# Performance work log

Measured on AMD Instinct MI355X. Metric: run time of the kernel, lower is better.

The kernel has to match this reference:

```python
import jax, jax.numpy as jnp
import numpy as np

IN_FEAT = 3 * 299 * 299  # 268203
D1 = 512
H = 28
OUT = 2


def setup_inputs() -> dict:
    key = jax.random.key(0)
    ks = jax.random.split(key, 10)
    B, T = 4, 64
    s1 = 1.0 / np.sqrt(IN_FEAT)
    s2 = 1.0 / np.sqrt(D1)
    s3 = 1.0 / np.sqrt(H)
    return {
        "x": jax.random.normal(ks[0], (B, T, 3, 299, 299), jnp.float32),
        "W1": jax.random.uniform(ks[1], (IN_FEAT, D1), jnp.float32, -s1, s1),
        "b1": jax.random.uniform(ks[2], (D1,), jnp.float32, -s1, s1),
        "Wi": jax.random.uniform(ks[3], (D1, H), jnp.float32, -s2, s2),
        "Wr": jax.random.uniform(ks[4], (H, H), jnp.float32, -s3, s3),
        "br": jax.random.uniform(ks[5], (H,), jnp.float32, -s3, s3),
        "A": jax.random.normal(ks[6], (H,), jnp.float32),
        "tau": 1.0 + jax.random.uniform(ks[7], (H,), jnp.float32),  # positive time constants
        "W2": jax.random.uniform(ks[8], (H, OUT), jnp.float32, -s3, s3),
        "b2": jax.random.uniform(ks[9], (OUT,), jnp.float32, -s3, s3),
    }


def reference(x, W1, b1, Wi, Wr, br, A, tau, W2, b2):
    B, T = x.shape[0], x.shape[1]
    xf = x.reshape(B, T, -1)                      # [B, T, 268203]
    h1 = jax.nn.relu(jnp.einsum('btf,fd->btd', xf, W1) + b1)  # [B, T, 512]
    u = jnp.einsum('btd,dh->bth', h1, Wi)         # precomputed input drive [B, T, H]
    dt = 1.0

    def step(h, u_t):
        # fused-Euler LTC cell: f gates both time-constant and attractor A
        ft = jax.nn.sigmoid(u_t + h @ Wr + br)
        h_new = (h + dt * ft * A) / (1.0 + dt * (1.0 / tau + ft))
        return h_new, h_new

    h0 = jnp.zeros((B, H), x.dtype)
    _, hs = jax.lax.scan(step, h0, jnp.swapaxes(u, 0, 1))  # [T, B, H]
    last = jax.nn.relu(hs[-1])                    # relu then take last step
    out = last @ W2 + b2                          # [B, 2]
    return jax.nn.sigmoid(out)
```

## Files before the change

### kernel.cpp

```cpp
#include <hip/hip_runtime.h>
#include <hip/hip_bf16.h>

#define KTOT   268203
#define MROWS  256
#define NCOLS  512
#define HDIM   28
#define NSTEPS 8382
#define FSTEP  8381
#define KREM   11
#define BN     256

typedef __attribute__((ext_vector_type(4))) float  f32x4;
typedef __attribute__((ext_vector_type(8))) __bf16 bf16x8;

#define AUX_NT 2

static __device__ inline bf16x8 pack8(const float* f) {
    union { bf16x8 v; __hip_bfloat16 h[8]; } u;
    #pragma unroll
    for (int j = 0; j < 8; ++j) u.h[j] = __float2bfloat16(f[j]);
    return u.v;
}
static __device__ inline unsigned short bfbits(float v) {
    __hip_bfloat16 h = __float2bfloat16(v);
    union { __hip_bfloat16 h; unsigned short u; } c; c.h = h; return c.u;
}

__global__ __launch_bounds__(512, 2) void gemm1_kernel(
    const float* __restrict__ x, const float* __restrict__ W1,
    __hip_bfloat16* __restrict__ part, int steps_per, int nks)
{
    __shared__ __align__(16) float Albuf[2][MROWS * 32];
    __shared__ __align__(16) float Bbuf[2][32 * BN];

    const int tid  = threadIdx.x;
    const int lane = tid & 63;
    const int w    = tid >> 6;
    const int wm   = w >> 1;
    const int wn   = w & 1;

    int bx, ks;
    {
        const int id = blockIdx.x;
        if ((nks & 7) == 0) {
            const int xcd = id & 7;
            const int m_  = id >> 3;
            bx = m_ & 1;
            ks = ((m_ >> 1) << 3) | xcd;
        } else {
            bx = id & 1;
            ks = id >> 1;
        }
    }
    const int bcol = bx * BN;

    const int dlt = lane >> 5;
    const int m   = lane & 31;
    const int rw7 = (2 * w + dlt) & 7;
    const int ag  = (m >> 2) ^ rw7;
    const size_t a_off = (size_t)(2 * w + dlt) * KTOT + ag * 4 + (m & 3);
    const size_t b_off = bcol + (size_t)(lane) * 4;

    f32x4 acc[4][8];
    #pragma unroll
    for (int i = 0; i < 4; ++i)
        #pragma unroll
        for (int j = 0; j < 8; ++j)
            acc[i][j] = (f32x4){0.f, 0.f, 0.f, 0.f};

    const int s0 = ks * steps_per;
    int s1 = s0 + steps_per;
    if (s1 > NSTEPS) s1 = NSTEPS;
    int s1f = (s1 < FSTEP) ? s1 : FSTEP;
    int nfull = s1f - s0;
    if (nfull < 0) nfull = 0;

    auto issue_step = [&](int s, int buf) {
        const float* ap = x + a_off + (size_t)s * 32;
        #pragma unroll
        for (int i = 0; i < 16; ++i) {
            const float* gp = ap + (size_t)i * 16 * KTOT;
            char* lp = (char*)&Albuf[buf][0] + (i * 8 + w) * 256;
            __builtin_amdgcn_global_load_lds(
                (const __attribute__((address_space(1))) unsigned int*)(const void*)gp,
                (__attribute__((address_space(3))) unsigned int*)(void*)lp, 4, 0, 0);
        }
        const float* bp = W1 + b_off + (size_t)s * 32 * NCOLS;
        #pragma unroll
        for (int i = 0; i < 4; ++i) {
            const float* gp = bp + (size_t)(i * 8 + w) * NCOLS;
            char* lp = (char*)&Bbuf[buf][0] + (i * 8 + w) * 1024;
            __builtin_amdgcn_global_load_lds(
                (const __attribute__((address_space(1))) unsigned int*)(const void*)gp,
                (__attribute__((address_space(3))) unsigned int*)(void*)lp, 16, 0, AUX_NT);
        }
    };

    auto compute = [&](int buf) {
        const int rc = lane & 15, ko = lane >> 4;
        bf16x8 bq[8];
        #pragma unroll
        for (int ni = 0; ni < 8; ++ni) {
            const int colL = wn * 128 + ni * 16 + rc;
            float bf[8];
            #pragma unroll
            for (int j = 0; j < 8; ++j)
                bf[j] = Bbuf[buf][(ko * 8 + j) * BN + colL];
            bq[ni] = pack8(bf);
        }
        const int soff = ((2 * ko) ^ (rc & 7)) * 16;
        #pragma unroll
        for (int mi = 0; mi < 4; ++mi) {
            const int ab = (wm * 64 + mi * 16 + rc) * 128;
            float afv[8];
            *(f32x4*)&afv[0] = *(const f32x4*)((const char*)&Albuf[buf][0] + ab + soff);
            *(f32x4*)&afv[4] = *(const f32x4*)((const char*)&Albuf[buf][0] + ab + (soff ^ 16));
            const bf16x8 af = pack8(afv);
            #pragma unroll
            for (int ni = 0; ni < 8; ++ni)
                acc[mi][ni] = __builtin_amdgcn_mfma_f32_16x16x32_bf16(
                    af, bq[ni], acc[mi][ni], 0, 0, 0);
        }
    };

    if (nfull > 0) {
        issue_step(s0, 0);
        if (nfull > 1) issue_step(s0 + 1, 1);
        for (int t = 0; t < nfull; ++t) {
            if (t + 1 < nfull) { asm volatile("s_waitcnt vmcnt(20)" ::: "memory"); }
            else               { asm volatile("s_waitcnt vmcnt(0)"  ::: "memory"); }
            __builtin_amdgcn_s_barrier();
            __builtin_amdgcn_sched_barrier(0);
            compute(t & 1);
            __builtin_amdgcn_sched_barrier(0);
            __builtin_amdgcn_s_barrier();
            if (t + 2 < nfull) issue_step(s0 + t + 2, t & 1);
        }
    }

    if (s1 > FSTEP && s0 < s1) {
        const int buf = nfull & 1;
        __syncthreads();
        {
            const int row = tid >> 1, half = tid & 1;
            #pragma unroll
            for (int i = 0; i < 16; ++i) {
                const int k = half * 16 + i;
                const float v = (k < KREM)
                    ? x[(size_t)row * KTOT + (size_t)FSTEP * 32 + k] : 0.f;
                Albuf[buf][row * 32 + ((k >> 2) ^ (row & 7)) * 4 + (k & 3)] = v;
            }
        }
        {
            const int c = tid & 255, og = tid >> 8;
            #pragma unroll
            for (int i = 0; i < 16; ++i) {
                const int k = og * 16 + i;
                const float v = (k < KREM)
                    ? W1[(size_t)(FSTEP * 32 + k) * NCOLS + bcol + c] : 0.f;
                Bbuf[buf][k * BN + c] = v;
            }
        }
        __syncthreads();
        compute(buf);
    }

    __hip_bfloat16* outp = part + (size_t)ks * MROWS * NCOLS;
    const int rc = lane & 15, q = lane >> 4;
    #pragma unroll
    for (int mi = 0; mi < 4; ++mi) {
        #pragma unroll
        for (int ni = 0; ni < 8; ++ni) {
            const int col = bcol + wn * 128 + ni * 16 + rc;
            #pragma unroll
            for (int j = 0; j < 4; ++j) {
                const int row = wm * 64 + mi * 16 + q * 4 + j;
                const float v  = acc[mi][ni][j];
                const float vh = __shfl_xor(v, 1);
                if (!(rc & 1)) {
                    const unsigned int pk =
                        (unsigned int)bfbits(v) | ((unsigned int)bfbits(vh) << 16);
                    *(unsigned int*)(outp + (size_t)row * NCOLS + col) = pk;
                }
            }
        }
    }
}

__global__ __launch_bounds__(512) void reduce_u_kernel(
    const __hip_bfloat16* __restrict__ part, const float* __restrict__ b1,
    const float* __restrict__ Wi, float* __restrict__ u, int nks)
{
    __shared__ float h1[NCOLS];
    __shared__ f32x4 red[4][128];
    const int row = blockIdx.x;
    const int tid = threadIdx.x;
    const int c4  = tid & 127;
    const int kk  = tid >> 7;

    const unsigned short* pu = (const unsigned short*)part;
    f32x4 sum = (f32x4){0.f, 0.f, 0.f, 0.f};
    for (int k = kk; k < nks; k += 4) {
        const size_t base = ((size_t)k * MROWS + row) * NCOLS + c4 * 4;
        ushort4 pv = *(const ushort4*)&pu[base];
        union { unsigned int u; float f; } c0, c1, c2, c3;
        c0.u = (unsigned int)pv.x << 16; c1.u = (unsigned int)pv.y << 16;
        c2.u = (unsigned int)pv.z << 16; c3.u = (unsigned int)pv.w << 16;
        sum[0] += c0.f; sum[1] += c1.f; sum[2] += c2.f; sum[3] += c3.f;
    }
    red[kk][c4] = sum;
    __syncthreads();

    if (tid < 128) {
        f32x4 t = red[0][tid] + red[1][tid] + red[2][tid] + red[3][tid];
        const f32x4 bb = *(const f32x4*)&b1[tid * 4];
        t += bb;
        #pragma unroll
        for (int j = 0; j < 4; ++j) h1[tid * 4 + j] = fmaxf(t[j], 0.f);
    }
    __syncthreads();

    const int wv = tid >> 6, lane = tid & 63;
    #pragma unroll
    for (int hh = 0; hh < 4; ++hh) {
        const int h = wv * 4 + hh;
        if (h < HDIM) {
            float p = 0.f;
            #pragma unroll
            for (int dd = 0; dd < 8; ++dd) {
                const int d = lane + dd * 64;
                p += h1[d] * Wi[d * HDIM + h];
            }
            #pragma unroll
            for (int off = 32; off; off >>= 1) p += __shfl_down(p, off);
            if (lane == 0) u[row * HDIM + h] = p;
        }
    }
}

__global__ __launch_bounds__(64) void recur_kernel(
    const float* __restrict__ u, const float* __restrict__ Wr,
    const float* __restrict__ br, const float* __restrict__ Av,
    const float* __restrict__ tau, const float* __restrict__ W2,
    const float* __restrict__ b2, float* __restrict__ out)
{
    const int b = blockIdx.x;
    const int j = threadIdx.x;
    const bool act = j < HDIM;
    const int jj = act ? j : 0;

    float wr[HDIM];
    #pragma unroll
    for (int i = 0; i < HDIM; ++i) wr[i] = act ? Wr[i * HDIM + jj] : 0.f;
    const float brj = act ? br[jj] : 0.f;
    const float Aj  = act ? Av[jj] : 0.f;
    const float itj = act ? (1.f / tau[jj]) : 0.f;

    float uv[64];
    #pragma unroll
    for (int t = 0; t < 64; ++t)
        uv[t] = act ? u[(b * 64 + t) * HDIM + jj] : 0.f;

    float h = 0.f;
    #pragma unroll
    for (int t = 0; t < 64; ++t) {
        float a = uv[t] + brj;
        #pragma unroll
        for (int i = 0; i < HDIM; ++i)
            a += __shfl(h, i) * wr[i];
        const float ft = 1.f / (1.f + expf(-a));
        const float hn = (h + ft * Aj) / (1.f + itj + ft);
        h = act ? hn : 0.f;
    }

    const float r  = act ? fmaxf(h, 0.f) : 0.f;
    float p0 = act ? r * W2[jj * 2 + 0] : 0.f;
    float p1 = act ? r * W2[jj * 2 + 1] : 0.f;
    #pragma unroll
    for (int off = 32; off; off >>= 1) {
        p0 += __shfl_down(p0, off);
        p1 += __shfl_down(p1, off);
    }
    if (j == 0) {
        out[b * 2 + 0] = 1.f / (1.f + expf(-(p0 + b2[0])));
        out[b * 2 + 1] = 1.f / (1.f + expf(-(p1 + b2[1])));
    }
}

extern "C" void kernel_launch(void* const* d_in, const int* in_sizes, int n_in,
                              void* d_out, int out_size, void* d_ws, size_t ws_size,
                              hipStream_t stream)
{
    (void)in_sizes; (void)n_in; (void)out_size;
    const float* x   = (const float*)d_in[0];
    const float* W1  = (const float*)d_in[1];
    const float* b1  = (const float*)d_in[2];
    const float* Wi  = (const float*)d_in[3];
    const float* Wr  = (const float*)d_in[4];
    const float* br  = (const float*)d_in[5];
    const float* Av  = (const float*)d_in[6];
    const float* tau = (const float*)d_in[7];
    const float* W2  = (const float*)d_in[8];
    const float* b2  = (const float*)d_in[9];
    float* out = (float*)d_out;

    const size_t per_split = (size_t)MROWS * NCOLS * sizeof(__hip_bfloat16);
    int nks = 128;
    while (nks > 8 && (size_t)nks * per_split + (1 << 16) > ws_size) nks >>= 1;
    const int steps_per = (NSTEPS + nks - 1) / nks;

    __hip_bfloat16* part = (__hip_bfloat16*)d_ws;
    float* u = (float*)((char*)d_ws + (size_t)nks * per_split);

    gemm1_kernel<<<dim3(2 * nks), 512, 0, stream>>>(x, W1, part, steps_per, nks);
    reduce_u_kernel<<<dim3(MROWS), 512, 0, stream>>>(part, b1, Wi, u, nks);
    recur_kernel<<<dim3(4), 64, 0, stream>>>(u, Wr, br, Av, tau, W2, b2, out);
}
```

Before: 285.0 us.

## Stage W1 tiles through registers as transposed bf16 in LDS

W1 tiles are now loaded into registers with ordinary global loads instead of direct global-to-LDS copies. They are converted to bf16 and written into a padded, column-major LDS layout (BROWS=40) so compute can read each B fragment with a single 16-byte LDS load instead of eight scalar reads plus packing. The main loop is unrolled by two so each half uses a fixed register bank and LDS buffer, and the vmcnt thresholds are adjusted to match. The change removes repeated float-to-bf16 conversion across waves and cuts LDS footprint and traffic. In exchange it adds register pressure, a register-to-LDS write stage before each barrier, and less asynchronous overlap for the B loads.

```diff
diff --git a/kernel.cpp b/kernel.cpp
--- a/kernel.cpp
+++ b/kernel.cpp
@@ -9,11 +9,11 @@
 #define FSTEP  8381
 #define KREM   11
 #define BN     256
-
-typedef __attribute__((ext_vector_type(4))) float  f32x4;
-typedef __attribute__((ext_vector_type(8))) __bf16 bf16x8;
-
-#define AUX_NT 2
+#define BROWS  40
+
+typedef __attribute__((ext_vector_type(4))) float        f32x4;
+typedef __attribute__((ext_vector_type(4))) unsigned int u32x4;
+typedef __attribute__((ext_vector_type(8))) __bf16       bf16x8;
 
 static __device__ inline bf16x8 pack8(const float* f) {
     union { bf16x8 v; __hip_bfloat16 h[8]; } u;
@@ -30,8 +30,8 @@
     const float* __restrict__ x, const float* __restrict__ W1,
     __hip_bfloat16* __restrict__ part, int steps_per, int nks)
 {
-    __shared__ __align__(16) float Albuf[2][MROWS * 32];
-    __shared__ __align__(16) float Bbuf[2][32 * BN];
+    __shared__ __align__(16) float          Albuf[2][MROWS * 32];
+    __shared__ __align__(16) __hip_bfloat16 Blds[2][BN * BROWS];
 
     const int tid  = threadIdx.x;
     const int lane = tid & 63;
@@ -59,7 +59,8 @@
     const int rw7 = (2 * w + dlt) & 7;
     const int ag  = (m >> 2) ^ rw7;
     const size_t a_off = (size_t)(2 * w + dlt) * KTOT + ag * 4 + (m & 3);
-    const size_t b_off = bcol + (size_t)(lane) * 4;
+    const int bkh  = w >> 2;
+    const int bcl  = (w & 3) * 64 + lane;
 
     f32x4 acc[4][8];
     #pragma unroll
@@ -75,7 +76,9 @@
     int nfull = s1f - s0;
     if (nfull < 0) nfull = 0;
 
-    auto issue_step = [&](int s, int buf) {
+    float bregA[16], bregB[16];
+
+    auto issueA = [&](int s, int buf) {
         const float* ap = x + a_off + (size_t)s * 32;
         #pragma unroll
         for (int i = 0; i < 16; ++i) {
@@ -85,29 +88,30 @@
                 (const __attribute__((address_space(1))) unsigned int*)(const void*)gp,
                 (__attribute__((address_space(3))) unsigned int*)(void*)lp, 4, 0, 0);
         }
-        const float* bp = W1 + b_off + (size_t)s * 32 * NCOLS;
-        #pragma unroll
-        for (int i = 0; i < 4; ++i) {
-            const float* gp = bp + (size_t)(i * 8 + w) * NCOLS;
-            char* lp = (char*)&Bbuf[buf][0] + (i * 8 + w) * 1024;
-            __builtin_amdgcn_global_load_lds(
-                (const __attribute__((address_space(1))) unsigned int*)(const void*)gp,
-                (__attribute__((address_space(3))) unsigned int*)(void*)lp, 16, 0, AUX_NT);
-        }
+    };
+    auto loadB = [&](int s, float* breg) {
+        const float* bp = W1 + ((size_t)s * 32 + bkh * 16) * NCOLS + bcol + bcl;
+        #pragma unroll
+        for (int kk = 0; kk < 16; ++kk)
+            breg[kk] = bp[(size_t)kk * NCOLS];
+    };
+    auto writeB = [&](const float* breg, int buf) {
+        unsigned int pk[8];
+        #pragma unroll
+        for (int q = 0; q < 8; ++q)
+            pk[q] = (unsigned int)bfbits(breg[2 * q]) |
+                    ((unsigned int)bfbits(breg[2 * q + 1]) << 16);
+        __hip_bfloat16* dst = &Blds[buf][bcl * BROWS + bkh * 16];
+        *(u32x4*)(dst)     = (u32x4){pk[0], pk[1], pk[2], pk[3]};
+        *(u32x4*)(dst + 8) = (u32x4){pk[4], pk[5], pk[6], pk[7]};
     };
 
     auto compute = [&](int buf) {
         const int rc = lane & 15, ko = lane >> 4;
         bf16x8 bq[8];
         #pragma unroll
-        for (int ni = 0; ni < 8; ++ni) {
-            const int colL = wn * 128 + ni * 16 + rc;
-            float bf[8];
-            #pragma unroll
-            for (int j = 0; j < 8; ++j)
-                bf[j] = Bbuf[buf][(ko * 8 + j) * BN + colL];
-            bq[ni] = pack8(bf);
-        }
+        for (int ni = 0; ni < 8; ++ni)
+            bq[ni] = *(const bf16x8*)&Blds[buf][(wn * 128 + ni * 16 + rc) * BROWS + ko * 8];
         const int soff = ((2 * ko) ^ (rc & 7)) * 16;
         #pragma unroll
         for (int mi = 0; mi < 4; ++mi) {
@@ -124,17 +128,36 @@
     };
 
     if (nfull > 0) {
-        issue_step(s0, 0);
-        if (nfull > 1) issue_step(s0 + 1, 1);
-        for (int t = 0; t < nfull; ++t) {
-            if (t + 1 < nfull) { asm volatile("s_waitcnt vmcnt(20)" ::: "memory"); }
+        issueA(s0, 0); loadB(s0, bregA);
+        if (nfull > 1) { issueA(s0 + 1, 1); loadB(s0 + 1, bregB); }
+        int t = 0;
+        for (;;) {
+            if (t + 1 < nfull) { asm volatile("s_waitcnt vmcnt(32)" ::: "memory"); }
             else               { asm volatile("s_waitcnt vmcnt(0)"  ::: "memory"); }
+            __builtin_amdgcn_sched_barrier(0);
+            writeB(bregA, 0);
+            asm volatile("s_waitcnt lgkmcnt(0)" ::: "memory");
+            __builtin_amdgcn_sched_barrier(0);
             __builtin_amdgcn_s_barrier();
             __builtin_amdgcn_sched_barrier(0);
-            compute(t & 1);
+            compute(0);
             __builtin_amdgcn_sched_barrier(0);
             __builtin_amdgcn_s_barrier();
-            if (t + 2 < nfull) issue_step(s0 + t + 2, t & 1);
+            if (t + 2 < nfull) { issueA(s0 + t + 2, 0); loadB(s0 + t + 2, bregA); }
+            if (++t >= nfull) break;
+            if (t + 1 < nfull) { asm volatile("s_waitcnt vmcnt(32)" ::: "memory"); }
+            else               { asm volatile("s_waitcnt vmcnt(0)"  ::: "memory"); }
+            __builtin_amdgcn_sched_barrier(0);
+            writeB(bregB, 1);
+            asm volatile("s_waitcnt lgkmcnt(0)" ::: "memory");
+            __builtin_amdgcn_sched_barrier(0);
+            __builtin_amdgcn_s_barrier();
+            __builtin_amdgcn_sched_barrier(0);
+            compute(1);
+            __builtin_amdgcn_sched_barrier(0);
+            __builtin_amdgcn_s_barrier();
+            if (t + 2 < nfull) { issueA(s0 + t + 2, 1); loadB(s0 + t + 2, bregB); }
+            if (++t >= nfull) break;
         }
     }
 
@@ -158,7 +181,7 @@
                 const int k = og * 16 + i;
                 const float v = (k < KREM)
                     ? W1[(size_t)(FSTEP * 32 + k) * NCOLS + bcol + c] : 0.f;
-                Bbuf[buf][k * BN + c] = v;
+                Blds[buf][c * BROWS + k] = __float2bfloat16(v);
             }
         }
         __syncthreads();
```

New measurement: 270.3 us. 5.2% less time.
